# Kernel tuning notes

Measured on AMD Instinct MI355X. Metric: run time of the kernel, lower is better.

Reference implementation:

```python
import jax, jax.numpy as jnp
import numpy as np
from math import sqrt

H = 16  # num_heads
E = 1024  # embedding_size
B, S = 2, 2048

def setup_inputs() -> dict:
    key = jax.random.key(0)
    ks = jax.random.split(key, 12)
    sc = 1.0 / sqrt(E)
    inp = {
        'q': jax.random.normal(ks[0], (B, S, E), jnp.float32),
        'k': jax.random.normal(ks[1], (B, S, E), jnp.float32),
        'v': jax.random.normal(ks[2], (B, S, E), jnp.float32),
        'Wq': jax.random.normal(ks[3], (E, E), jnp.float32) * sc,
        'bq': jnp.zeros((E,), jnp.float32),
        'Wk': jax.random.normal(ks[4], (E, E), jnp.float32) * sc,
        'bk': jnp.zeros((E,), jnp.float32),
        'Wv': jax.random.normal(ks[5], (E, E), jnp.float32) * sc,
        'bv': jnp.zeros((E,), jnp.float32),
        'Wo': jax.random.normal(ks[6], (E, E), jnp.float32) * sc,
        'bo': jnp.zeros((E,), jnp.float32),
        'gamma': jnp.ones((E,), jnp.float32),
        'beta': jnp.zeros((E,), jnp.float32),
        'attn_mask': jnp.tril(jnp.ones((S, S), jnp.int32))[None, None],  # causal [1,1,S,S]
        'pad_mask': jnp.ones((B, S), jnp.int32),
    }
    return inp


def reference(q, k, v, Wq, bq, Wk, bk, Wv, bv, Wo, bo, gamma, beta, attn_mask, pad_mask):
    hs = E // H
    residual = q
    # NOTE: faithful to original: contiguous view(-1, H, S, hs) reinterprets
    # [B, S, E] memory directly as [B, H, S, hs] (no transpose).
    qh = (q @ Wq + bq).reshape(B, H, S, hs)
    kh = (k @ Wk + bk).reshape(B, H, S, hs)
    vh = (v @ Wv + bv).reshape(B, H, S, hs)
    scores = jnp.einsum('bhqd,bhkd->bhqk', qh, kh)  # [B,H,Sq,Sk]
    neg_inf = jnp.float32(-jnp.inf)
    scores = jnp.where(pad_mask[:, None, None, :] == 0, neg_inf, scores)
    scores = jnp.where(attn_mask == 0, neg_inf, scores)
    attn = jax.nn.softmax(scores / sqrt(hs), axis=-1)
    out = jnp.einsum('bhqk,bhkd->bhqd', attn, vh).reshape(B, S, E)
    out = out @ Wo + bo  # dropout is identity at inference
    x = residual + out
    mean = jnp.mean(x, axis=-1, keepdims=True)
    std = jnp.sqrt(jnp.mean((x - mean) ** 2, axis=-1, keepdims=True))  # unbiased=False
    return gamma * ((x - mean) / (std + 1e-8)) + beta
```

## Files before the change

kernel.cpp:

```cpp
#include <hip/hip_runtime.h>
#include <hip/hip_bf16.h>
#include <stdint.h>
#include <math.h>

#define NH 16
#define E_ 1024
#define B_ 2
#define S_ 2048
#define HS 64
#define M_TOT (B_*S_)

typedef __attribute__((ext_vector_type(4))) float f32x4;
typedef __attribute__((ext_vector_type(8))) short short8;

static __device__ __forceinline__ short f2bf(float f) {
    union { __hip_bfloat16 h; short s; } u;
    u.h = __float2bfloat16(f);
    return u.s;
}

static __device__ __forceinline__ void glds16(const void* g, void* l) {
    __builtin_amdgcn_global_load_lds(
        (__attribute__((address_space(1))) void*)(g),
        (__attribute__((address_space(3))) void*)(l),
        16, 0, 0);
}

__global__ __launch_bounds__(256) void prep(
    const float* __restrict__ q, const float* __restrict__ k, const float* __restrict__ v,
    const float* __restrict__ Wq, const float* __restrict__ Wk,
    const float* __restrict__ Wv, const float* __restrict__ Wo,
    short* __restrict__ qb, short* __restrict__ kb, short* __restrict__ vb,
    short* __restrict__ Wqt, short* __restrict__ Wkt,
    short* __restrict__ Wvt, short* __restrict__ Wot)
{
    __shared__ float tile[32][33];
    const int id  = blockIdx.x;
    const int tid = threadIdx.x;
    if (id < 4096) {
        const int m = id >> 10, t = id & 1023;
        const int n0 = (t & 31) * 32, k0 = (t >> 5) * 32;
        const float* W; short* Wt;
        switch (m) {
            case 0: W = Wq; Wt = Wqt; break;
            case 1: W = Wk; Wt = Wkt; break;
            case 2: W = Wv; Wt = Wvt; break;
            default: W = Wo; Wt = Wot; break;
        }
        const int tx = tid & 31, ty = tid >> 5;
#pragma unroll
        for (int i = 0; i < 4; i++)
            tile[ty + 8*i][tx] = W[(size_t)(k0 + ty + 8*i) * E_ + n0 + tx];
        __syncthreads();
#pragma unroll
        for (int i = 0; i < 4; i++)
            Wt[(size_t)(n0 + ty + 8*i) * E_ + k0 + tx] = f2bf(tile[tx][ty + 8*i]);
    } else {
        const int idx = id - 4096;
        const int tensor = idx >> 12;
        const int blk = idx & 4095;
        const float* src = (tensor == 0) ? q : (tensor == 1) ? k : v;
        short* dst = (tensor == 0) ? qb : (tensor == 1) ? kb : vb;
        const int i = (blk * 256 + tid) * 4;
        float4 f = *(const float4*)(src + i);
        short4 o;
        o.x = f2bf(f.x); o.y = f2bf(f.y); o.z = f2bf(f.z); o.w = f2bf(f.w);
        *(short4*)(dst + i) = o;
    }
}

__global__ __launch_bounds__(256) void transpose_v(
    const short* __restrict__ Vb, short* __restrict__ Vt_g)
{
    __shared__ short tile[64][68];
    const int bh = blockIdx.z;
    const int s0 = blockIdx.x * 64;
    const int t  = threadIdx.x;
    const int rr = t >> 4;
    const int cc = (t & 15) * 4;
    const short* src = Vb + ((size_t)bh * S_ + s0) * HS;
#pragma unroll
    for (int p = 0; p < 4; p++) {
        uint2 d2 = *(const uint2*)(src + (size_t)(rr + 16*p) * HS + cc);
        *(uint2*)(&tile[rr + 16*p][cc]) = d2;
    }
    __syncthreads();
    short* dst = Vt_g + (size_t)bh * HS * S_;
#pragma unroll
    for (int p = 0; p < 4; p++) {
        const int d = rr + 16*p;
        short4 o;
        o.x = tile[cc+0][d];
        o.y = tile[cc+1][d];
        o.z = tile[cc+2][d];
        o.w = tile[cc+3][d];
        *(short4*)(dst + (size_t)d * S_ + s0 + cc) = o;
    }
}

#define BM 128
#define BN 128
#define BK 32

template<int MODE>
__device__ __forceinline__ void gemm_core(
    const short* __restrict__ A, const short* __restrict__ Bt,
    const float* __restrict__ bias,
    short* __restrict__ outb, float* __restrict__ outf,
    int mblk, int nblk, int kbeg, int kend)
{
    __shared__ __align__(16) short As[BM * BK];
    __shared__ __align__(16) short Bs[BN * BK];

    const int tid  = threadIdx.x;
    const int lane = tid & 63;
    const int w    = tid >> 6;
    const int wm   = w >> 1, wn = w & 1;
    const int l15  = lane & 15, quad = lane >> 4;
    const int N = E_, K = E_;

    f32x4 acc[4][4];
#pragma unroll
    for (int i = 0; i < 4; i++)
#pragma unroll
        for (int j = 0; j < 4; j++)
            acc[i][j] = (f32x4){0.f, 0.f, 0.f, 0.f};

    const int arow = tid >> 2;
    const int acol = (tid & 3) * 8;
    const int m0 = mblk * BM, n0 = nblk * BN;
    short* AsW0 = As + w * 512;
    short* AsW1 = As + 2048 + w * 512;
    short* BsW0 = Bs + w * 512;
    short* BsW1 = Bs + 2048 + w * 512;

    for (int k0 = kbeg; k0 < kend; k0 += BK) {
        __syncthreads();
        glds16(A  + (size_t)(m0 + arow)      * K + k0 + acol, AsW0);
        glds16(A  + (size_t)(m0 + arow + 64) * K + k0 + acol, AsW1);
        glds16(Bt + (size_t)(n0 + arow)      * K + k0 + acol, BsW0);
        glds16(Bt + (size_t)(n0 + arow + 64) * K + k0 + acol, BsW1);
        __syncthreads();

        short8 af[4], bf[4];
#pragma unroll
        for (int i = 0; i < 4; i++)
            af[i] = *(const short8*)(As + (wm*64 + i*16 + l15) * BK + quad*8);
#pragma unroll
        for (int j = 0; j < 4; j++)
            bf[j] = *(const short8*)(Bs + (wn*64 + j*16 + l15) * BK + quad*8);
#pragma unroll
        for (int i = 0; i < 4; i++)
#pragma unroll
            for (int j = 0; j < 4; j++)
                acc[i][j] = __builtin_amdgcn_mfma_f32_16x16x32_bf16(af[i], bf[j], acc[i][j], 0, 0, 0);
    }

#pragma unroll
    for (int i = 0; i < 4; i++)
#pragma unroll
        for (int j = 0; j < 4; j++) {
            int col = n0 + wn*64 + j*16 + l15;
            float bcol = (MODE == 0) ? bias[col] : 0.f;
#pragma unroll
            for (int r = 0; r < 4; r++) {
                int row = m0 + wm*64 + i*16 + quad*4 + r;
                if (MODE == 0) {
                    outb[(size_t)row * N + col] = f2bf(acc[i][j][r] + bcol);
                } else {
                    outf[(size_t)row * N + col] = acc[i][j][r];
                }
            }
        }
}

__global__ __launch_bounds__(256) void gemm_qkv(
    const short* qb, const short* kb, const short* vb,
    const short* Wqt, const short* Wkt, const short* Wvt,
    const float* bq, const float* bk, const float* bv,
    short* Qb, short* Kb, short* Vb)
{
    const short *A, *Bt; const float* bias; short* out;
    switch (blockIdx.z) {
        case 0:  A = qb; Bt = Wqt; bias = bq; out = Qb; break;
        case 1:  A = kb; Bt = Wkt; bias = bk; out = Kb; break;
        default: A = vb; Bt = Wvt; bias = bv; out = Vb; break;
    }
    gemm_core<0>(A, Bt, bias, out, nullptr, blockIdx.x, blockIdx.y, 0, E_);
}

__global__ __launch_bounds__(256) void gemm_out_sk(
    const short* Ab, const short* Wot, float* xb0, float* xb1)
{
    float* out = (blockIdx.z == 0) ? xb0 : xb1;
    int kbeg = blockIdx.z * (E_ / 2);
    gemm_core<1>(Ab, Wot, nullptr, nullptr, out, blockIdx.x, blockIdx.y, kbeg, kbeg + E_/2);
}

#define SP  72
#define SPP 68

__global__ __launch_bounds__(256, 4) void flash_attn(
    const short* __restrict__ Q, const short* __restrict__ K,
    const short* __restrict__ Vt_g, short* __restrict__ O)
{
    const int bh  = blockIdx.x;
    const int qy  = blockIdx.y;
    const int ua  = qy & 7, ub = qy >> 3;
    const int qt  = (ub == 0) ? ua : (ub == 1) ? 15 - ua : (ub == 2) ? 16 + ua : 31 - ua;
    const int tid = threadIdx.x;
    const int lane = tid & 63, w = tid >> 6;
    const int l15 = lane & 15, quad = lane >> 4;

    __shared__ __align__(16) short Ks[64 * SP];
    __shared__ __align__(16) short Vt[64 * SP];
    __shared__ __align__(16) short Ps[4][16 * SPP];
    short* myPs = Ps[w];

    const short* Qbase = Q + ((size_t)bh * S_ + qt * 64 + w * 16) * HS;
    const short* Kb0   = K + (size_t)bh * S_ * HS;
    const short* Vg    = Vt_g + (size_t)bh * HS * S_;

    const int r0 = tid >> 3, c0 = (tid & 7) * 8;
    const int r1 = (tid + 256) >> 3, c1 = c0;

    short8 qf[2];
    qf[0] = *(const short8*)(Qbase + l15 * HS + quad * 8);
    qf[1] = *(const short8*)(Qbase + l15 * HS + 32 + quad * 8);

    uint4 rk0, rk1, rv0, rv1;
    {
        const short* Kt = Kb0;
        rk0 = *(const uint4*)(Kt + tid * 8);
        rk1 = *(const uint4*)(Kt + (tid + 256) * 8);
        rv0 = *(const uint4*)(Vg + (size_t)r0 * S_ + c0);
        rv1 = *(const uint4*)(Vg + (size_t)r1 * S_ + c1);
    }

    f32x4 o_acc[4];
#pragma unroll
    for (int j = 0; j < 4; j++) o_acc[j] = (f32x4){0.f, 0.f, 0.f, 0.f};
    float lsum[4] = {0.f, 0.f, 0.f, 0.f};

    const float SCL = 0.125f * 1.44269504088896341f;

    for (int kt = 0; kt <= qt; kt++) {
        __syncthreads();
        *(uint4*)(Ks + r0 * SP + c0) = rk0;
        *(uint4*)(Ks + r1 * SP + c1) = rk1;
        *(uint4*)(Vt + r0 * SP + c0) = rv0;
        *(uint4*)(Vt + r1 * SP + c1) = rv1;
        __syncthreads();

        if (kt < qt) {
            const short* Kt = Kb0 + (size_t)(kt + 1) * 64 * HS;
            rk0 = *(const uint4*)(Kt + tid * 8);
            rk1 = *(const uint4*)(Kt + (tid + 256) * 8);
            rv0 = *(const uint4*)(Vg + (size_t)r0 * S_ + (kt + 1) * 64 + c0);
            rv1 = *(const uint4*)(Vg + (size_t)r1 * S_ + (kt + 1) * 64 + c1);
        }

        f32x4 sc[4];
#pragma unroll
        for (int j = 0; j < 4; j++) sc[j] = (f32x4){0.f, 0.f, 0.f, 0.f};
        __builtin_amdgcn_s_setprio(1);
#pragma unroll
        for (int ks = 0; ks < 2; ks++)
#pragma unroll
            for (int j = 0; j < 4; j++) {
                short8 bk_ = *(const short8*)(Ks + (j*16 + l15) * SP + ks*32 + quad*8);
                sc[j] = __builtin_amdgcn_mfma_f32_16x16x32_bf16(qf[ks], bk_, sc[j], 0, 0, 0);
            }
        __builtin_amdgcn_s_setprio(0);

        const bool diag = (kt == qt);
#pragma unroll
        for (int r = 0; r < 4; r++) {
            int qrow = w*16 + quad*4 + r;
            float rs = 0.f;
#pragma unroll
            for (int j = 0; j < 4; j++) {
                float p = exp2f(sc[j][r] * SCL);
                if (diag) { int kc = j*16 + l15; if (kc > qrow) p = 0.f; }
                rs += p;
                myPs[(quad*4 + r) * SPP + j*16 + l15] = f2bf(p);
            }
            lsum[r] += rs;
        }

        short8 ap[2];
        ap[0] = *(const short8*)(myPs + l15 * SPP + quad*8);
        ap[1] = *(const short8*)(myPs + l15 * SPP + 32 + quad*8);
        __builtin_amdgcn_s_setprio(1);
#pragma unroll
        for (int ks = 0; ks < 2; ks++)
#pragma unroll
            for (int j2 = 0; j2 < 4; j2++) {
                short8 bv_ = *(const short8*)(Vt + (j2*16 + l15) * SP + ks*32 + quad*8);
                o_acc[j2] = __builtin_amdgcn_mfma_f32_16x16x32_bf16(ap[ks], bv_, o_acc[j2], 0, 0, 0);
            }
        __builtin_amdgcn_s_setprio(0);
    }

#pragma unroll
    for (int r = 0; r < 4; r++) {
#pragma unroll
        for (int off = 1; off < 16; off <<= 1)
            lsum[r] += __shfl_xor(lsum[r], off);
    }

    short* Ob = O + ((size_t)bh * S_ + qt * 64 + w * 16) * HS;
#pragma unroll
    for (int r = 0; r < 4; r++) {
        float inv = 1.f / lsum[r];
#pragma unroll
        for (int j2 = 0; j2 < 4; j2++)
            Ob[(quad*4 + r) * HS + j2*16 + l15] = f2bf(o_acc[j2][r] * inv);
    }
}

__global__ __launch_bounds__(256) void layernorm_k(
    const float* __restrict__ xb0, const float* __restrict__ xb1,
    const float* __restrict__ resid, const float* __restrict__ bo,
    const float* __restrict__ gamma, const float* __restrict__ beta,
    float* __restrict__ out)
{
    int row = blockIdx.x;
    int tid = threadIdx.x;
    size_t o4 = (size_t)row * E_ + tid * 4;
    float4 a = *(const float4*)(xb0 + o4);
    float4 b2 = *(const float4*)(xb1 + o4);
    float4 c = *(const float4*)(resid + o4);
    float4 d = *(const float4*)(bo + tid * 4);
    float4 v;
    v.x = a.x + b2.x + c.x + d.x;
    v.y = a.y + b2.y + c.y + d.y;
    v.z = a.z + b2.z + c.z + d.z;
    v.w = a.w + b2.w + c.w + d.w;

    float s = v.x + v.y + v.z + v.w;
#pragma unroll
    for (int off = 1; off < 64; off <<= 1) s += __shfl_xor(s, off);
    __shared__ float red[4];
    if ((tid & 63) == 0) red[tid >> 6] = s;
    __syncthreads();
    float mean = (red[0] + red[1] + red[2] + red[3]) * (1.f / E_);

    float dx0 = v.x - mean, dx1 = v.y - mean, dx2 = v.z - mean, dx3 = v.w - mean;
    float sq = dx0*dx0 + dx1*dx1 + dx2*dx2 + dx3*dx3;
#pragma unroll
    for (int off = 1; off < 64; off <<= 1) sq += __shfl_xor(sq, off);
    __syncthreads();
    if ((tid & 63) == 0) red[tid >> 6] = sq;
    __syncthreads();
    float var = (red[0] + red[1] + red[2] + red[3]) * (1.f / E_);
    float inv = 1.f / (sqrtf(var) + 1e-8f);

    float4 g = *(const float4*)(gamma + tid * 4);
    float4 b = *(const float4*)(beta + tid * 4);
    float4 o;
    o.x = g.x * dx0 * inv + b.x;
    o.y = g.y * dx1 * inv + b.y;
    o.z = g.z * dx2 * inv + b.z;
    o.w = g.w * dx3 * inv + b.w;
    *(float4*)(out + o4) = o;
}

extern "C" void kernel_launch(void* const* d_in, const int* in_sizes, int n_in,
                              void* d_out, int out_size, void* d_ws, size_t ws_size,
                              hipStream_t stream)
{
    const float* q     = (const float*)d_in[0];
    const float* k     = (const float*)d_in[1];
    const float* v     = (const float*)d_in[2];
    const float* Wq    = (const float*)d_in[3];
    const float* bq    = (const float*)d_in[4];
    const float* Wk    = (const float*)d_in[5];
    const float* bk    = (const float*)d_in[6];
    const float* Wv    = (const float*)d_in[7];
    const float* bv    = (const float*)d_in[8];
    const float* Wo    = (const float*)d_in[9];
    const float* bo    = (const float*)d_in[10];
    const float* gamma = (const float*)d_in[11];
    const float* beta  = (const float*)d_in[12];

    const size_t ACT = (size_t)M_TOT * E_;
    char* ws = (char*)d_ws;
    size_t off = 0;
    auto alloc = [&](size_t bytes) { char* p = ws + off; off += bytes; return p; };

    short* Wqt  = (short*)alloc((size_t)E_ * E_ * 2);
    short* Wkt  = (short*)alloc((size_t)E_ * E_ * 2);
    short* Wvt  = (short*)alloc((size_t)E_ * E_ * 2);
    short* Wot  = (short*)alloc((size_t)E_ * E_ * 2);
    short* qb   = (short*)alloc(ACT * 2);
    short* kb   = (short*)alloc(ACT * 2);
    short* vb   = (short*)alloc(ACT * 2);
    short* Qb   = (short*)alloc(ACT * 2);
    short* Kb   = (short*)alloc(ACT * 2);
    short* Vb   = (short*)alloc(ACT * 2);
    short* Vt_g = (short*)alloc(ACT * 2);
    short* Ob   = (short*)alloc(ACT * 2);
    float* xb0  = (float*)alloc(ACT * 4);
    float* xb1  = (float*)Qb;

    prep<<<16384, 256, 0, stream>>>(q, k, v, Wq, Wk, Wv, Wo,
                                    qb, kb, vb, Wqt, Wkt, Wvt, Wot);
    gemm_qkv<<<dim3(M_TOT / BM, E_ / BN, 3), 256, 0, stream>>>(qb, kb, vb, Wqt, Wkt, Wvt,
                                                               bq, bk, bv, Qb, Kb, Vb);
    transpose_v<<<dim3(S_ / 64, 1, B_ * NH), 256, 0, stream>>>(Vb, Vt_g);
    flash_attn<<<dim3(B_ * NH, S_ / 64), 256, 0, stream>>>(Qb, Kb, Vt_g, Ob);
    gemm_out_sk<<<dim3(M_TOT / BM, E_ / BN, 2), 256, 0, stream>>>(Ob, Wot, xb0, xb1);
    layernorm_k<<<M_TOT, 256, 0, stream>>>(xb0, xb1, q, bo, gamma, beta, (float*)d_out);
}
```

Baseline: 263.9 us.

## Process two 64-row query tiles per flash-attention block to reuse K/V tiles

Each flash-attention block now handles 128 query rows as two 64-row halves. Every K/V tile staged in shared memory is used by both halves, which halves the global-to-LDS traffic and barrier count per query row, and the grid shrinks accordingly. The cost is more registers: occupancy drops to 2 blocks per SIMD budget, there are fewer blocks for load balancing, and the setprio hints are gone.

```diff
diff --git a/kernel.cpp b/kernel.cpp
--- a/kernel.cpp
+++ b/kernel.cpp
@@ -200,14 +200,14 @@
 #define SP  72
 #define SPP 68
 
-__global__ __launch_bounds__(256, 4) void flash_attn(
+__global__ __launch_bounds__(256, 2) void flash_attn(
     const short* __restrict__ Q, const short* __restrict__ K,
     const short* __restrict__ Vt_g, short* __restrict__ O)
 {
     const int bh  = blockIdx.x;
     const int qy  = blockIdx.y;
     const int ua  = qy & 7, ub = qy >> 3;
-    const int qt  = (ub == 0) ? ua : (ub == 1) ? 15 - ua : (ub == 2) ? 16 + ua : 31 - ua;
+    const int qt  = (ub == 0) ? ua : 15 - ua;
     const int tid = threadIdx.x;
     const int lane = tid & 63, w = tid >> 6;
     const int l15 = lane & 15, quad = lane >> 4;
@@ -217,34 +217,40 @@
     __shared__ __align__(16) short Ps[4][16 * SPP];
     short* myPs = Ps[w];
 
-    const short* Qbase = Q + ((size_t)bh * S_ + qt * 64 + w * 16) * HS;
-    const short* Kb0   = K + (size_t)bh * S_ * HS;
-    const short* Vg    = Vt_g + (size_t)bh * HS * S_;
+    const short* Kb0 = K + (size_t)bh * S_ * HS;
+    const short* Vg  = Vt_g + (size_t)bh * HS * S_;
 
     const int r0 = tid >> 3, c0 = (tid & 7) * 8;
     const int r1 = (tid + 256) >> 3, c1 = c0;
 
-    short8 qf[2];
-    qf[0] = *(const short8*)(Qbase + l15 * HS + quad * 8);
-    qf[1] = *(const short8*)(Qbase + l15 * HS + 32 + quad * 8);
-
-    uint4 rk0, rk1, rv0, rv1;
+    short8 qf[2][2];
     {
-        const short* Kt = Kb0;
-        rk0 = *(const uint4*)(Kt + tid * 8);
-        rk1 = *(const uint4*)(Kt + (tid + 256) * 8);
-        rv0 = *(const uint4*)(Vg + (size_t)r0 * S_ + c0);
-        rv1 = *(const uint4*)(Vg + (size_t)r1 * S_ + c1);
-    }
-
-    f32x4 o_acc[4];
-#pragma unroll
-    for (int j = 0; j < 4; j++) o_acc[j] = (f32x4){0.f, 0.f, 0.f, 0.f};
-    float lsum[4] = {0.f, 0.f, 0.f, 0.f};
+        const short* Qb_ = Q + ((size_t)bh * S_ + qt * 128 + w * 16) * HS;
+        qf[0][0] = *(const short8*)(Qb_ + l15 * HS + quad * 8);
+        qf[0][1] = *(const short8*)(Qb_ + l15 * HS + 32 + quad * 8);
+        qf[1][0] = *(const short8*)(Qb_ + (size_t)64 * HS + l15 * HS + quad * 8);
+        qf[1][1] = *(const short8*)(Qb_ + (size_t)64 * HS + l15 * HS + 32 + quad * 8);
+    }
+
+    uint4 rk0 = *(const uint4*)(Kb0 + tid * 8);
+    uint4 rk1 = *(const uint4*)(Kb0 + (tid + 256) * 8);
+    uint4 rv0 = *(const uint4*)(Vg + (size_t)r0 * S_ + c0);
+    uint4 rv1 = *(const uint4*)(Vg + (size_t)r1 * S_ + c1);
+
+    f32x4 o_acc[2][4];
+    float lsum[2][4];
+#pragma unroll
+    for (int h = 0; h < 2; h++)
+#pragma unroll
+        for (int j = 0; j < 4; j++) {
+            o_acc[h][j] = (f32x4){0.f, 0.f, 0.f, 0.f};
+            lsum[h][j] = 0.f;
+        }
 
     const float SCL = 0.125f * 1.44269504088896341f;
-
-    for (int kt = 0; kt <= qt; kt++) {
+    const int ktmax = 2 * qt + 1;
+
+    for (int kt = 0; kt <= ktmax; kt++) {
         __syncthreads();
         *(uint4*)(Ks + r0 * SP + c0) = rk0;
         *(uint4*)(Ks + r1 * SP + c1) = rk1;
@@ -252,7 +258,7 @@
         *(uint4*)(Vt + r1 * SP + c1) = rv1;
         __syncthreads();
 
-        if (kt < qt) {
+        if (kt < ktmax) {
             const short* Kt = Kb0 + (size_t)(kt + 1) * 64 * HS;
             rk0 = *(const uint4*)(Kt + tid * 8);
             rk1 = *(const uint4*)(Kt + (tid + 256) * 8);
@@ -260,62 +266,65 @@
             rv1 = *(const uint4*)(Vg + (size_t)r1 * S_ + (kt + 1) * 64 + c1);
         }
 
-        f32x4 sc[4];
-#pragma unroll
-        for (int j = 0; j < 4; j++) sc[j] = (f32x4){0.f, 0.f, 0.f, 0.f};
-        __builtin_amdgcn_s_setprio(1);
-#pragma unroll
-        for (int ks = 0; ks < 2; ks++)
-#pragma unroll
-            for (int j = 0; j < 4; j++) {
-                short8 bk_ = *(const short8*)(Ks + (j*16 + l15) * SP + ks*32 + quad*8);
-                sc[j] = __builtin_amdgcn_mfma_f32_16x16x32_bf16(qf[ks], bk_, sc[j], 0, 0, 0);
+#pragma unroll
+        for (int h = 0; h < 2; h++) {
+            if (kt > 2 * qt + h) continue;
+
+            f32x4 sc[4];
+#pragma unroll
+            for (int j = 0; j < 4; j++) sc[j] = (f32x4){0.f, 0.f, 0.f, 0.f};
+#pragma unroll
+            for (int ks = 0; ks < 2; ks++)
+#pragma unroll
+                for (int j = 0; j < 4; j++) {
+                    short8 bk_ = *(const short8*)(Ks + (j*16 + l15) * SP + ks*32 + quad*8);
+                    sc[j] = __builtin_amdgcn_mfma_f32_16x16x32_bf16(qf[h][ks], bk_, sc[j], 0, 0, 0);
+                }
+
+            const bool diag = (kt == 2 * qt + h);
+#pragma unroll
+            for (int r = 0; r < 4; r++) {
+                int qrow = w*16 + quad*4 + r;
+                float rs = 0.f;
+#pragma unroll
+                for (int j = 0; j < 4; j++) {
+                    float p = exp2f(sc[j][r] * SCL);
+                    if (diag) { int kc = j*16 + l15; if (kc > qrow) p = 0.f; }
+                    rs += p;
+                    myPs[(quad*4 + r) * SPP + j*16 + l15] = f2bf(p);
+                }
+                lsum[h][r] += rs;
             }
-        __builtin_amdgcn_s_setprio(0);
-
-        const bool diag = (kt == qt);
+
+            short8 ap[2];
+            ap[0] = *(const short8*)(myPs + l15 * SPP + quad*8);
+            ap[1] = *(const short8*)(myPs + l15 * SPP + 32 + quad*8);
+#pragma unroll
+            for (int ks = 0; ks < 2; ks++)
+#pragma unroll
+                for (int j2 = 0; j2 < 4; j2++) {
+                    short8 bv_ = *(const short8*)(Vt + (j2*16 + l15) * SP + ks*32 + quad*8);
+                    o_acc[h][j2] = __builtin_amdgcn_mfma_f32_16x16x32_bf16(ap[ks], bv_, o_acc[h][j2], 0, 0, 0);
+                }
+        }
+    }
+
+#pragma unroll
+    for (int h = 0; h < 2; h++) {
 #pragma unroll
         for (int r = 0; r < 4; r++) {
-            int qrow = w*16 + quad*4 + r;
-            float rs = 0.f;
-#pragma unroll
-            for (int j = 0; j < 4; j++) {
-                float p = exp2f(sc[j][r] * SCL);
-                if (diag) { int kc = j*16 + l15; if (kc > qrow) p = 0.f; }
-                rs += p;
-                myPs[(quad*4 + r) * SPP + j*16 + l15] = f2bf(p);
-            }
-            lsum[r] += rs;
-        }
-
-        short8 ap[2];
-        ap[0] = *(const short8*)(myPs + l15 * SPP + quad*8);
-        ap[1] = *(const short8*)(myPs + l15 * SPP + 32 + quad*8);
-        __builtin_amdgcn_s_setprio(1);
-#pragma unroll
-        for (int ks = 0; ks < 2; ks++)
-#pragma unroll
-            for (int j2 = 0; j2 < 4; j2++) {
-                short8 bv_ = *(const short8*)(Vt + (j2*16 + l15) * SP + ks*32 + quad*8);
-                o_acc[j2] = __builtin_amdgcn_mfma_f32_16x16x32_bf16(ap[ks], bv_, o_acc[j2], 0, 0, 0);
-            }
-        __builtin_amdgcn_s_setprio(0);
-    }
-
-#pragma unroll
-    for (int r = 0; r < 4; r++) {
-#pragma unroll
-        for (int off = 1; off < 16; off <<= 1)
-            lsum[r] += __shfl_xor(lsum[r], off);
-    }
-
-    short* Ob = O + ((size_t)bh * S_ + qt * 64 + w * 16) * HS;
-#pragma unroll
-    for (int r = 0; r < 4; r++) {
-        float inv = 1.f / lsum[r];
-#pragma unroll
-        for (int j2 = 0; j2 < 4; j2++)
-            Ob[(quad*4 + r) * HS + j2*16 + l15] = f2bf(o_acc[j2][r] * inv);
+#pragma unroll
+            for (int off = 1; off < 16; off <<= 1)
+                lsum[h][r] += __shfl_xor(lsum[h][r], off);
+        }
+        short* Ob = O + ((size_t)bh * S_ + qt * 128 + h * 64 + w * 16) * HS;
+#pragma unroll
+        for (int r = 0; r < 4; r++) {
+            float inv = 1.f / lsum[h][r];
+#pragma unroll
+            for (int j2 = 0; j2 < 4; j2++)
+                Ob[(quad*4 + r) * HS + j2*16 + l15] = f2bf(o_acc[h][j2][r] * inv);
+        }
     }
 }
 
@@ -409,7 +418,7 @@
     gemm_qkv<<<dim3(M_TOT / BM, E_ / BN, 3), 256, 0, stream>>>(qb, kb, vb, Wqt, Wkt, Wvt,
                                                                bq, bk, bv, Qb, Kb, Vb);
     transpose_v<<<dim3(S_ / 64, 1, B_ * NH), 256, 0, stream>>>(Vb, Vt_g);
-    flash_attn<<<dim3(B_ * NH, S_ / 64), 256, 0, stream>>>(Qb, Kb, Vt_g, Ob);
+    flash_attn<<<dim3(B_ * NH, S_ / 128), 256, 0, stream>>>(Qb, Kb, Vt_g, Ob);
     gemm_out_sk<<<dim3(M_TOT / BM, E_ / BN, 2), 256, 0, stream>>>(Ob, Wot, xb0, xb1);
     layernorm_k<<<M_TOT, 256, 0, stream>>>(xb0, xb1, q, bo, gamma, beta, (float*)d_out);
 }
```

Measured after the change: 287.9 us. 1.09x slower.

## Double-buffer K/V tiles in LDS for flash attention

Applied to the files above, without the earlier changes.

Splits the K and V shared-memory tiles into two buffers so the next tile is written to LDS while the current one is used by the MFMAs. This removes one __syncthreads per key tile, and the first tile is staged before the loop. The s_setprio hints around the MFMA loops are dropped and launch bounds go from 4 to 3 blocks per CU. The larger LDS footprint lowers the possible occupancy of the attention kernel, which may offset the saved barrier.

```diff
diff --git a/kernel.cpp b/kernel.cpp
--- a/kernel.cpp
+++ b/kernel.cpp
@@ -200,7 +200,7 @@
 #define SP  72
 #define SPP 68
 
-__global__ __launch_bounds__(256, 4) void flash_attn(
+__global__ __launch_bounds__(256, 3) void flash_attn(
     const short* __restrict__ Q, const short* __restrict__ K,
     const short* __restrict__ Vt_g, short* __restrict__ O)
 {
@@ -212,8 +212,8 @@
     const int lane = tid & 63, w = tid >> 6;
     const int l15 = lane & 15, quad = lane >> 4;
 
-    __shared__ __align__(16) short Ks[64 * SP];
-    __shared__ __align__(16) short Vt[64 * SP];
+    __shared__ __align__(16) short Ks[2][64 * SP];
+    __shared__ __align__(16) short Vt[2][64 * SP];
     __shared__ __align__(16) short Ps[4][16 * SPP];
     short* myPs = Ps[w];
 
@@ -228,13 +228,20 @@
     qf[0] = *(const short8*)(Qbase + l15 * HS + quad * 8);
     qf[1] = *(const short8*)(Qbase + l15 * HS + 32 + quad * 8);
 
-    uint4 rk0, rk1, rv0, rv1;
-    {
-        const short* Kt = Kb0;
+    uint4 rk0 = *(const uint4*)(Kb0 + tid * 8);
+    uint4 rk1 = *(const uint4*)(Kb0 + (tid + 256) * 8);
+    uint4 rv0 = *(const uint4*)(Vg + (size_t)r0 * S_ + c0);
+    uint4 rv1 = *(const uint4*)(Vg + (size_t)r1 * S_ + c1);
+    *(uint4*)(&Ks[0][r0 * SP + c0]) = rk0;
+    *(uint4*)(&Ks[0][r1 * SP + c1]) = rk1;
+    *(uint4*)(&Vt[0][r0 * SP + c0]) = rv0;
+    *(uint4*)(&Vt[0][r1 * SP + c1]) = rv1;
+    if (qt > 0) {
+        const short* Kt = Kb0 + (size_t)64 * HS;
         rk0 = *(const uint4*)(Kt + tid * 8);
         rk1 = *(const uint4*)(Kt + (tid + 256) * 8);
-        rv0 = *(const uint4*)(Vg + (size_t)r0 * S_ + c0);
-        rv1 = *(const uint4*)(Vg + (size_t)r1 * S_ + c1);
+        rv0 = *(const uint4*)(Vg + (size_t)r0 * S_ + 64 + c0);
+        rv1 = *(const uint4*)(Vg + (size_t)r1 * S_ + 64 + c1);
     }
 
     f32x4 o_acc[4];
@@ -245,33 +252,35 @@
     const float SCL = 0.125f * 1.44269504088896341f;
 
     for (int kt = 0; kt <= qt; kt++) {
+        const int cur = kt & 1;
         __syncthreads();
-        *(uint4*)(Ks + r0 * SP + c0) = rk0;
-        *(uint4*)(Ks + r1 * SP + c1) = rk1;
-        *(uint4*)(Vt + r0 * SP + c0) = rv0;
-        *(uint4*)(Vt + r1 * SP + c1) = rv1;
-        __syncthreads();
 
         if (kt < qt) {
-            const short* Kt = Kb0 + (size_t)(kt + 1) * 64 * HS;
-            rk0 = *(const uint4*)(Kt + tid * 8);
-            rk1 = *(const uint4*)(Kt + (tid + 256) * 8);
-            rv0 = *(const uint4*)(Vg + (size_t)r0 * S_ + (kt + 1) * 64 + c0);
-            rv1 = *(const uint4*)(Vg + (size_t)r1 * S_ + (kt + 1) * 64 + c1);
+            *(uint4*)(&Ks[cur ^ 1][r0 * SP + c0]) = rk0;
+            *(uint4*)(&Ks[cur ^ 1][r1 * SP + c1]) = rk1;
+            *(uint4*)(&Vt[cur ^ 1][r0 * SP + c0]) = rv0;
+            *(uint4*)(&Vt[cur ^ 1][r1 * SP + c1]) = rv1;
+            if (kt + 1 < qt) {
+                const short* Kt = Kb0 + (size_t)(kt + 2) * 64 * HS;
+                rk0 = *(const uint4*)(Kt + tid * 8);
+                rk1 = *(const uint4*)(Kt + (tid + 256) * 8);
+                rv0 = *(const uint4*)(Vg + (size_t)r0 * S_ + (kt + 2) * 64 + c0);
+                rv1 = *(const uint4*)(Vg + (size_t)r1 * S_ + (kt + 2) * 64 + c1);
+            }
         }
 
+        const short* Kc = Ks[cur];
+        const short* Vc = Vt[cur];
         f32x4 sc[4];
 #pragma unroll
         for (int j = 0; j < 4; j++) sc[j] = (f32x4){0.f, 0.f, 0.f, 0.f};
-        __builtin_amdgcn_s_setprio(1);
 #pragma unroll
         for (int ks = 0; ks < 2; ks++)
 #pragma unroll
             for (int j = 0; j < 4; j++) {
-                short8 bk_ = *(const short8*)(Ks + (j*16 + l15) * SP + ks*32 + quad*8);
+                short8 bk_ = *(const short8*)(Kc + (j*16 + l15) * SP + ks*32 + quad*8);
                 sc[j] = __builtin_amdgcn_mfma_f32_16x16x32_bf16(qf[ks], bk_, sc[j], 0, 0, 0);
             }
-        __builtin_amdgcn_s_setprio(0);
 
         const bool diag = (kt == qt);
 #pragma unroll
@@ -291,15 +300,13 @@
         short8 ap[2];
         ap[0] = *(const short8*)(myPs + l15 * SPP + quad*8);
         ap[1] = *(const short8*)(myPs + l15 * SPP + 32 + quad*8);
-        __builtin_amdgcn_s_setprio(1);
 #pragma unroll
         for (int ks = 0; ks < 2; ks++)
 #pragma unroll
             for (int j2 = 0; j2 < 4; j2++) {
-                short8 bv_ = *(const short8*)(Vt + (j2*16 + l15) * SP + ks*32 + quad*8);
+                short8 bv_ = *(const short8*)(Vc + (j2*16 + l15) * SP + ks*32 + quad*8);
                 o_acc[j2] = __builtin_amdgcn_mfma_f32_16x16x32_bf16(ap[ks], bv_, o_acc[j2], 0, 0, 0);
             }
-        __builtin_amdgcn_s_setprio(0);
     }
 
 #pragma unroll
```

After: 263.1 us. Within noise of the previous version (-0.3%).
